# Optimization experiments

Measured on AMD Instinct MI355X. Metric: run time of the kernel, lower is better.

## Reference

```python
import jax, jax.numpy as jnp
import numpy as np
import math

B, H, S, D = 4, 16, 2048, 128

def setup_inputs() -> dict:
    key = jax.random.key(0)
    kq, kk, kv = jax.random.split(key, 3)
    query = jax.random.normal(kq, (B, H, S, D), dtype=jnp.float32)
    k = jax.random.normal(kk, (B, H, S, D), dtype=jnp.float32)
    value = jax.random.normal(kv, (B, H, S, D), dtype=jnp.float32)
    attn_mask = jnp.tril(jnp.ones((S, S), dtype=bool))  # causal
    key_padding_mask = jnp.ones((B, S), dtype=bool)      # all keys valid
    return {"query": query, "key": k, "value": value,
            "attn_mask": attn_mask, "key_padding_mask": key_padding_mask}

def reference(query, key, value, attn_mask, key_padding_mask):
    dk = query.shape[-1]
    # [B,H,Sq,Sk]
    scores = jnp.einsum('bhqd,bhkd->bhqk', query, key) / math.sqrt(dk)
    fill = jnp.finfo(scores.dtype).min
    # attn_mask [Sq,Sk] -> [1,1,Sq,Sk]; True = keep
    scores = jnp.where(attn_mask[None, None, :, :], scores, fill)
    # key_padding_mask [B,Sk] -> [B,1,1,Sk]; True = keep
    scores = jnp.where(key_padding_mask[:, None, None, :], scores, fill)
    attn = jax.nn.softmax(scores, axis=-1)
    # dropout p=0.0 / eval mode -> identity
    return jnp.einsum('bhqk,bhkd->bhqd', attn, value)
```

## Files before the change

### kernel.cpp

```cpp
#include <hip/hip_runtime.h>
#include <hip/hip_bf16.h>
#include <math.h>

#define S_LEN 2048
#define D_DIM 128
#define NHEADS 64

typedef unsigned short u16;
typedef __attribute__((ext_vector_type(8))) short bf16x8;
typedef __attribute__((ext_vector_type(4))) float f32x4;
typedef __attribute__((ext_vector_type(16))) float f32x16;

__device__ __forceinline__ u16 f2b(float f) {
  union { float f; unsigned u; } v; v.f = f;
  return (u16)((v.u + 0x7fffu + ((v.u >> 16) & 1u)) >> 16);
}
__device__ __forceinline__ unsigned cvtpk(float lo, float hi) {
  unsigned r;
  asm("v_cvt_pk_bf16_f32 %0, %1, %2" : "=v"(r) : "v"(lo), "v"(hi));
  return r;
}
__device__ __forceinline__ void pl32swap(unsigned &a, unsigned &b) {
  asm("v_permlane32_swap_b32 %0, %1" : "+v"(a), "+v"(b));
}
__device__ __forceinline__ f32x16 z16() {
  f32x16 v;
  #pragma unroll
  for (int i = 0; i < 16; ++i) v[i] = 0.f;
  return v;
}

#define GLL16(g, l) __builtin_amdgcn_global_load_lds(                       \
    (const __attribute__((address_space(1))) unsigned*)(g),                 \
    (__attribute__((address_space(3))) unsigned*)(l), 16, 0, 0)

__global__ __launch_bounds__(256, 2)
void conv_kernel(const float* __restrict__ K, const float* __restrict__ V,
                 u16* __restrict__ Kws, u16* __restrict__ Vws) {
  __shared__ float VLf[128 * 65];
  const int h = blockIdx.x >> 3;
  const int s = blockIdx.x & 7;
  const int tid = threadIdx.x;
  const size_t hb = (size_t)h * S_LEN * D_DIM;
  const float* Kb = K + hb;
  const float* Vb = V + hb;
  u16* Ko = Kws + hb;
  u16* Vo = Vws + hb;

  #pragma unroll 2
  for (int it = 0; it < 16; ++it) {
    int idx = it * 256 + tid;
    int k = 256 * s + (idx >> 4), g = idx & 15;
    const float* src = Kb + (size_t)k * D_DIM + 8 * g;
    float4 a = *(const float4*)src;
    float4 b = *(const float4*)(src + 4);
    bf16x8 f;
    f[0]=f2b(a.x); f[1]=f2b(a.y); f[2]=f2b(a.z); f[3]=f2b(a.w);
    f[4]=f2b(b.x); f[5]=f2b(b.y); f[6]=f2b(b.z); f[7]=f2b(b.w);
    *(bf16x8*)&Ko[(size_t)k * D_DIM + 8 * g] = f;
  }
  for (int tt = 0; tt < 4; ++tt) {
    const int k0t = 256 * s + 64 * tt;
    __syncthreads();
    #pragma unroll 2
    for (int it = 0; it < 8; ++it) {
      int idx = it * 256 + tid;
      int row = idx >> 5, c4 = idx & 31;
      float4 v = *(const float4*)(Vb + (size_t)(k0t + row) * D_DIM + 4 * c4);
      VLf[(4*c4 + 0) * 65 + row] = v.x;
      VLf[(4*c4 + 1) * 65 + row] = v.y;
      VLf[(4*c4 + 2) * 65 + row] = v.z;
      VLf[(4*c4 + 3) * 65 + row] = v.w;
    }
    __syncthreads();
    #pragma unroll
    for (int it = 0; it < 4; ++it) {
      int idx = it * 256 + tid;
      int d = idx >> 3, kc = idx & 7;
      const float* src = &VLf[d * 65 + 8 * kc];
      bf16x8 f;
      #pragma unroll
      for (int j = 0; j < 8; ++j) f[j] = f2b(src[j]);
      *(bf16x8*)&Vo[(size_t)d * S_LEN + k0t + 8 * kc] = f;
    }
  }
}

__global__ __launch_bounds__(512, 2)
void fattn8w(const float* __restrict__ Qg, const u16* __restrict__ Kws,
             const u16* __restrict__ Vws, float* __restrict__ Og) {
  __shared__ __align__(16) u16 Kl[3][8192];
  __shared__ __align__(16) u16 Vl[3][8192];

  const int tid = threadIdx.x, lane = tid & 63, w = tid >> 6;
  const int l31 = lane & 31, hi = lane >> 5;
  const int kx = l31 & 7;

  const int L = blockIdx.x;
  const int xcd = L & 7, slot = L >> 3;
  const int head = xcd * 8 + (slot >> 2);
  const int pr = slot & 3;

  const size_t hb = (size_t)head * S_LEN * D_DIM;
  const float* Qb = Qg + hb;
  float*       Ob = Og + hb;
  const u16*   Kh = Kws + hb;
  const u16*   Vh = Vws + hb;

  auto stage = [&](int buf, int t) {
    const int k0 = t * 64;
    #pragma unroll
    for (int j = 0; j < 2; ++j) {
      const int sb = (w * 2 + j) * 64;
      {
        int sk = sb + lane;
        int k = sk >> 4, gs = sk & 15, g = gs ^ (k & 7);
        GLL16(Kh + (size_t)(k0 + k) * D_DIM + 8 * g, &Kl[buf][sb * 8]);
      }
      {
        int sv = sb + lane;
        int d = sv >> 3, gks = sv & 7, gk = gks ^ (d & 7);
        GLL16(Vh + (size_t)d * S_LEN + k0 + 8 * gk, &Vl[buf][sb * 8]);
      }
    }
  };

#define CHUNK(SV, CB, CI)                                                   \
  do {                                                                      \
    float p0 = exp2f((SV)[(CB)+0] - m_run), p1 = exp2f((SV)[(CB)+1] - m_run); \
    float p2 = exp2f((SV)[(CB)+2] - m_run), p3 = exp2f((SV)[(CB)+3] - m_run); \
    float p4 = exp2f((SV)[(CB)+4] - m_run), p5 = exp2f((SV)[(CB)+5] - m_run); \
    float p6 = exp2f((SV)[(CB)+6] - m_run), p7 = exp2f((SV)[(CB)+7] - m_run); \
    psA += (p0 + p1) + (p2 + p3);                                           \
    psB += (p4 + p5) + (p6 + p7);                                           \
    unsigned a0 = cvtpk(p0, p1), a1 = cvtpk(p2, p3);                        \
    unsigned a2 = cvtpk(p4, p5), a3 = cvtpk(p6, p7);                        \
    pl32swap(a0, a2); pl32swap(a1, a3);                                     \
    union { unsigned u[4]; bf16x8 v; } pf_;                                 \
    pf_.u[0] = a0; pf_.u[1] = a1; pf_.u[2] = a2; pf_.u[3] = a3;             \
    const int gv = ((CI) * 2 + hi) ^ kx;                                    \
    bf16x8 v0 = *(const bf16x8*)&V8[( l31      ) * 64 + gv * 8];            \
    bf16x8 v1 = *(const bf16x8*)&V8[( 32 + l31 ) * 64 + gv * 8];            \
    bf16x8 v2 = *(const bf16x8*)&V8[( 64 + l31 ) * 64 + gv * 8];            \
    bf16x8 v3 = *(const bf16x8*)&V8[( 96 + l31 ) * 64 + gv * 8];            \
    __builtin_amdgcn_s_setprio(1);                                          \
    oa0 = __builtin_amdgcn_mfma_f32_32x32x16_bf16(v0, pf_.v, oa0, 0,0,0);   \
    oa1 = __builtin_amdgcn_mfma_f32_32x32x16_bf16(v1, pf_.v, oa1, 0,0,0);   \
    oa2 = __builtin_amdgcn_mfma_f32_32x32x16_bf16(v2, pf_.v, oa2, 0,0,0);   \
    oa3 = __builtin_amdgcn_mfma_f32_32x32x16_bf16(v3, pf_.v, oa3, 0,0,0);   \
    __builtin_amdgcn_s_setprio(0);                                          \
  } while (0)

  #pragma unroll 1
  for (int qi = 0; qi < 2; ++qi) {
    const int qt  = qi ? pr : (7 - pr);
    const int q0w = qt * 256 + 32 * w;
    const int ntk = 4 * qt + 4;
    const int myq = q0w + l31;

    bf16x8 qf[8];
    {
      const float sc = 0.12753139f;
      const float* qp = Qb + (size_t)myq * D_DIM + 8 * hi;
      #pragma unroll
      for (int c = 0; c < 8; ++c) {
        float4 a = *(const float4*)(qp + 16 * c);
        float4 b = *(const float4*)(qp + 16 * c + 4);
        bf16x8 f;
        f[0]=f2b(a.x*sc); f[1]=f2b(a.y*sc); f[2]=f2b(a.z*sc); f[3]=f2b(a.w*sc);
        f[4]=f2b(b.x*sc); f[5]=f2b(b.y*sc); f[6]=f2b(b.z*sc); f[7]=f2b(b.w*sc);
        qf[c] = f;
      }
    }

    f32x16 oa0 = z16(), oa1 = z16(), oa2 = z16(), oa3 = z16();
    float m_run = 0.f, l_run = 0.f;

    stage(0, 0);
    stage(1, 1);
    int rb = 0;

    #pragma unroll 1
    for (int t = 0; t < ntk; ++t) {
      if (t + 1 < ntk) asm volatile("s_waitcnt vmcnt(4)" ::: "memory");
      else             asm volatile("s_waitcnt vmcnt(0)" ::: "memory");
      __builtin_amdgcn_s_barrier();
      asm volatile("" ::: "memory");

      if (64 * t <= q0w + 31) {
        const u16* K8 = &Kl[rb][0];
        const u16* V8 = &Vl[rb][0];

        f32x16 s0 = z16(), s1 = z16();
        __builtin_amdgcn_s_setprio(1);
        #pragma unroll
        for (int c = 0; c < 8; ++c) {
          const int gs = (c * 2 + hi) ^ kx;
          bf16x8 ka = *(const bf16x8*)&K8[ l31       * 128 + gs * 8];
          bf16x8 kb = *(const bf16x8*)&K8[(32 + l31) * 128 + gs * 8];
          s0 = __builtin_amdgcn_mfma_f32_32x32x16_bf16(ka, qf[c], s0, 0,0,0);
          s1 = __builtin_amdgcn_mfma_f32_32x32x16_bf16(kb, qf[c], s1, 0,0,0);
        }
        __builtin_amdgcn_s_setprio(0);

        if (64 * t + 63 > q0w) {
          const int qm = myq - 64 * t;
          #pragma unroll
          for (int i = 0; i < 16; ++i) {
            const int kr = (i & 3) + 8 * (i >> 2) + 4 * hi;
            if (kr > qm)      s0[i] = -1e30f;
            if (32 + kr > qm) s1[i] = -1e30f;
          }
        }

        float tm[16];
        #pragma unroll
        for (int i = 0; i < 16; ++i) tm[i] = fmaxf(s0[i], s1[i]);
        #pragma unroll
        for (int st = 8; st >= 1; st >>= 1)
          #pragma unroll
          for (int i = 0; i < 8; ++i) if (i < st) tm[i] = fmaxf(tm[i], tm[i+st]);
        float mx = fmaxf(tm[0], __shfl_xor(tm[0], 32));

        if (mx > m_run + 8.0f) {
          float corr = exp2f(m_run - mx);
          #pragma unroll
          for (int i = 0; i < 16; ++i) {
            oa0[i] *= corr; oa1[i] *= corr; oa2[i] *= corr; oa3[i] *= corr;
          }
          l_run *= corr; m_run = mx;
        }

        float psA = 0.f, psB = 0.f;
        CHUNK(s0, 0, 0);
        CHUNK(s0, 8, 1);
        CHUNK(s1, 0, 2);
        CHUNK(s1, 8, 3);
        l_run += psA + psB;
      }

      if (t + 2 < ntk) {
        int nb = rb + 2; if (nb >= 3) nb -= 3;
        stage(nb, t + 2);
      }
      asm volatile("" ::: "memory");
      rb = (rb + 1 == 3) ? 0 : rb + 1;
    }

    float l_tot = l_run + __shfl_xor(l_run, 32);
    float inv = 1.0f / l_tot;
    float* op = Ob + (size_t)myq * D_DIM;
    #pragma unroll
    for (int i = 0; i < 16; ++i) {
      const int d = (i & 3) + 8 * (i >> 2) + 4 * hi;
      op[d]      = oa0[i] * inv;
      op[32 + d] = oa1[i] * inv;
      op[64 + d] = oa2[i] * inv;
      op[96 + d] = oa3[i] * inv;
    }
    __builtin_amdgcn_s_barrier();
  }
#undef CHUNK
}

__global__ __launch_bounds__(256, 3)
void fattn_v2(const float* __restrict__ Qg, const float* __restrict__ Kg,
              const float* __restrict__ Vg, float* __restrict__ Og) {
  __shared__ __align__(16) u16 K8[16 * 64 * 8];
  __shared__ __align__(16) u16 V8[8 * 128 * 8];
  __shared__ __align__(16) u16 Plf[4 * 16 * 72];
  const int tid = threadIdx.x, lane = tid & 63, w = tid >> 6;
  const int lr = lane & 15, lg = lane >> 4;
  const int qtile = blockIdx.x % 32, bh = blockIdx.x / 32;
  const int q0 = qtile * 64;
  const size_t base = (size_t)bh * S_LEN * D_DIM;
  const float *Qb = Qg + base, *Kb = Kg + base, *Vb = Vg + base;
  float* Ob = Og + base;
  bf16x8 qf[4];
  {
    const float* qp = Qb + (size_t)(q0 + w * 16 + lr) * D_DIM + lg * 8;
    #pragma unroll
    for (int cc = 0; cc < 4; ++cc) {
      float4 a = *(const float4*)(qp + cc * 32);
      float4 b = *(const float4*)(qp + cc * 32 + 4);
      bf16x8 f;
      f[0]=f2b(a.x); f[1]=f2b(a.y); f[2]=f2b(a.z); f[3]=f2b(a.w);
      f[4]=f2b(b.x); f[5]=f2b(b.y); f[6]=f2b(b.z); f[7]=f2b(b.w);
      qf[cc] = f;
    }
  }
  f32x4 oacc[8];
  #pragma unroll
  for (int c = 0; c < 8; ++c) oacc[c] = (f32x4){0.f,0.f,0.f,0.f};
  float m_run[4] = {-INFINITY,-INFINITY,-INFINITY,-INFINITY};
  float l_run[4] = {0.f,0.f,0.f,0.f};
  const int sg_ = tid >> 5, dq_ = tid & 31;
  float4 kb[8], vb[8];
  auto prefetch = [&](int k0) {
    const float* kp = Kb + (size_t)(k0 + lane) * D_DIM;
    #pragma unroll
    for (int i = 0; i < 4; ++i) {
      int dg = w + 4 * i;
      kb[2*i]   = *(const float4*)(kp + dg * 8);
      kb[2*i+1] = *(const float4*)(kp + dg * 8 + 4);
    }
    #pragma unroll
    for (int jj = 0; jj < 8; ++jj) {
      int row = k0 + (jj & 3) * 16 + 2 * sg_ + (jj >> 2);
      vb[jj] = *(const float4*)(Vb + (size_t)row * D_DIM + dq_ * 4);
    }
  };
  const int ntiles = qtile + 1;
  const float scale = 0.08838834764831845f;
  prefetch(0);
  for (int t = 0; t < ntiles; ++t) {
    #pragma unroll
    for (int i = 0; i < 4; ++i) {
      int dg = w + 4 * i;
      float4 a = kb[2*i], b = kb[2*i+1];
      bf16x8 f;
      f[0]=f2b(a.x); f[1]=f2b(a.y); f[2]=f2b(a.z); f[3]=f2b(a.w);
      f[4]=f2b(b.x); f[5]=f2b(b.y); f[6]=f2b(b.z); f[7]=f2b(b.w);
      *(bf16x8*)&K8[(dg * 64 + lane) * 8] = f;
    }
    #pragma unroll
    for (int dd = 0; dd < 4; ++dd) {
      bf16x8 f;
      #pragma unroll
      for (int jj = 0; jj < 8; ++jj) {
        float c = (dd==0)?vb[jj].x:(dd==1)?vb[jj].y:(dd==2)?vb[jj].z:vb[jj].w;
        f[jj] = f2b(c);
      }
      *(bf16x8*)&V8[(sg_ * 128 + dq_ * 4 + dd) * 8] = f;
    }
    __syncthreads();
    if (t + 1 < ntiles) prefetch((t + 1) * 64);
    const bool diag = (t == qtile);
    f32x4 sa[4];
    #pragma unroll
    for (int c = 0; c < 4; ++c) sa[c] = (f32x4){0.f,0.f,0.f,0.f};
    #pragma unroll
    for (int cc = 0; cc < 4; ++cc) {
      #pragma unroll
      for (int c = 0; c < 4; ++c) {
        bf16x8 kf = *(const bf16x8*)&K8[((cc*4+lg)*64 + c*16 + lr)*8];
        sa[c] = __builtin_amdgcn_mfma_f32_16x16x32_bf16(qf[cc], kf, sa[c], 0,0,0);
      }
    }
    #pragma unroll
    for (int r = 0; r < 4; ++r) {
      float s0=sa[0][r]*scale, s1=sa[1][r]*scale, s2=sa[2][r]*scale, s3=sa[3][r]*scale;
      if (diag) {
        int lim = 16*w + lg*4 + r;
        if (     lr > lim) s0 = -INFINITY;
        if (16 + lr > lim) s1 = -INFINITY;
        if (32 + lr > lim) s2 = -INFINITY;
        if (48 + lr > lim) s3 = -INFINITY;
      }
      float mx = fmaxf(fmaxf(s0,s1), fmaxf(s2,s3));
      #pragma unroll
      for (int d = 1; d < 16; d <<= 1) mx = fmaxf(mx, __shfl_xor(mx, d));
      float mn = fmaxf(m_run[r], mx);
      float corr = __expf(m_run[r] - mn);
      float p0=__expf(s0-mn), p1=__expf(s1-mn), p2=__expf(s2-mn), p3=__expf(s3-mn);
      float ps = (p0+p1)+(p2+p3);
      #pragma unroll
      for (int d = 1; d < 16; d <<= 1) ps += __shfl_xor(ps, d);
      l_run[r] = l_run[r]*corr + ps;
      m_run[r] = mn;
      #pragma unroll
      for (int c = 0; c < 8; ++c) oacc[c][r] *= corr;
      ushort4 pw = make_ushort4(f2b(p0), f2b(p1), f2b(p2), f2b(p3));
      *(ushort4*)&Plf[((w*16 + lg*4 + r) * 72) + 4*lr] = pw;
    }
    #pragma unroll
    for (int pass = 0; pass < 2; ++pass) {
      bf16x8 pfv = *(const bf16x8*)&Plf[(w*16 + lr)*72 + pass*32 + lg*8];
      #pragma unroll
      for (int c = 0; c < 8; ++c) {
        bf16x8 vf = *(const bf16x8*)&V8[((pass*4 + lg)*128 + c*16 + lr)*8];
        oacc[c] = __builtin_amdgcn_mfma_f32_16x16x32_bf16(pfv, vf, oacc[c], 0,0,0);
      }
    }
    __syncthreads();
  }
  #pragma unroll
  for (int r = 0; r < 4; ++r) {
    const int mq = q0 + w*16 + lg*4 + r;
    const float inv = 1.0f / l_run[r];
    float* op = Ob + (size_t)mq * D_DIM + lr;
    #pragma unroll
    for (int c = 0; c < 8; ++c) op[c*16] = oacc[c][r] * inv;
  }
}

extern "C" void kernel_launch(void* const* d_in, const int* in_sizes, int n_in,
                              void* d_out, int out_size, void* d_ws, size_t ws_size,
                              hipStream_t stream) {
  const float* Q = (const float*)d_in[0];
  const float* K = (const float*)d_in[1];
  const float* V = (const float*)d_in[2];
  float* O = (float*)d_out;
  const size_t elems = (size_t)NHEADS * S_LEN * D_DIM;
  const size_t need = 2 * elems * sizeof(u16);
  if (ws_size >= need) {
    u16* Kws = (u16*)d_ws;
    u16* Vws = Kws + elems;
    conv_kernel<<<dim3(512), dim3(256), 0, stream>>>(K, V, Kws, Vws);
    fattn8w<<<dim3(256), dim3(512), 0, stream>>>(Q, Kws, Vws, O);
  } else {
    fattn_v2<<<dim3(NHEADS * 32), dim3(256), 0, stream>>>(Q, K, V, O);
  }
}
```

Baseline: 147.6 us.

## Switch to double-buffered 128-key tiles with two 64-key subtiles per barrier

```diff
diff --git a/kernel.cpp b/kernel.cpp
--- a/kernel.cpp
+++ b/kernel.cpp
@@ -89,8 +89,8 @@
 __global__ __launch_bounds__(512, 2)
 void fattn8w(const float* __restrict__ Qg, const u16* __restrict__ Kws,
              const u16* __restrict__ Vws, float* __restrict__ Og) {
-  __shared__ __align__(16) u16 Kl[3][8192];
-  __shared__ __align__(16) u16 Vl[3][8192];
+  __shared__ __align__(16) u16 Kl[2][16384];
+  __shared__ __align__(16) u16 Vl[2][16384];
 
   const int tid = threadIdx.x, lane = tid & 63, w = tid >> 6;
   const int l31 = lane & 31, hi = lane >> 5;
@@ -108,10 +108,10 @@
   const u16*   Vh = Vws + hb;
 
   auto stage = [&](int buf, int t) {
-    const int k0 = t * 64;
-    #pragma unroll
-    for (int j = 0; j < 2; ++j) {
-      const int sb = (w * 2 + j) * 64;
+    const int k0 = t * 128;
+    #pragma unroll
+    for (int j = 0; j < 4; ++j) {
+      const int sb = (w * 4 + j) * 64;
       {
         int sk = sb + lane;
         int k = sk >> 4, gs = sk & 15, g = gs ^ (k & 7);
@@ -119,13 +119,13 @@
       }
       {
         int sv = sb + lane;
-        int d = sv >> 3, gks = sv & 7, gk = gks ^ (d & 7);
+        int d = sv >> 4, gks = sv & 15, gk = gks ^ (d & 7);
         GLL16(Vh + (size_t)d * S_LEN + k0 + 8 * gk, &Vl[buf][sb * 8]);
       }
     }
   };
 
-#define CHUNK(SV, CB, CI)                                                   \
+#define CHUNK(SV, CB, CI, TS)                                               \
   do {                                                                      \
     float p0 = exp2f((SV)[(CB)+0] - m_run), p1 = exp2f((SV)[(CB)+1] - m_run); \
     float p2 = exp2f((SV)[(CB)+2] - m_run), p3 = exp2f((SV)[(CB)+3] - m_run); \
@@ -138,11 +138,11 @@
     pl32swap(a0, a2); pl32swap(a1, a3);                                     \
     union { unsigned u[4]; bf16x8 v; } pf_;                                 \
     pf_.u[0] = a0; pf_.u[1] = a1; pf_.u[2] = a2; pf_.u[3] = a3;             \
-    const int gv = ((CI) * 2 + hi) ^ kx;                                    \
-    bf16x8 v0 = *(const bf16x8*)&V8[( l31      ) * 64 + gv * 8];            \
-    bf16x8 v1 = *(const bf16x8*)&V8[( 32 + l31 ) * 64 + gv * 8];            \
-    bf16x8 v2 = *(const bf16x8*)&V8[( 64 + l31 ) * 64 + gv * 8];            \
-    bf16x8 v3 = *(const bf16x8*)&V8[( 96 + l31 ) * 64 + gv * 8];            \
+    const int gv8 = (((CI) * 2 + hi) ^ kx) * 8 + (TS) * 64;                 \
+    bf16x8 v0 = *(const bf16x8*)&V8[( l31      ) * 128 + gv8];              \
+    bf16x8 v1 = *(const bf16x8*)&V8[( 32 + l31 ) * 128 + gv8];              \
+    bf16x8 v2 = *(const bf16x8*)&V8[( 64 + l31 ) * 128 + gv8];              \
+    bf16x8 v3 = *(const bf16x8*)&V8[( 96 + l31 ) * 128 + gv8];              \
     __builtin_amdgcn_s_setprio(1);                                          \
     oa0 = __builtin_amdgcn_mfma_f32_32x32x16_bf16(v0, pf_.v, oa0, 0,0,0);   \
     oa1 = __builtin_amdgcn_mfma_f32_32x32x16_bf16(v1, pf_.v, oa1, 0,0,0);   \
@@ -151,12 +151,63 @@
     __builtin_amdgcn_s_setprio(0);                                          \
   } while (0)
 
+#define SUBTILE(TS)                                                         \
+  do {                                                                      \
+    const int kk0 = 128 * t + 64 * (TS);                                    \
+    if (kk0 <= q0w + 31) {                                                  \
+      f32x16 s0 = z16(), s1 = z16();                                        \
+      __builtin_amdgcn_s_setprio(1);                                        \
+      _Pragma("unroll")                                                     \
+      for (int c = 0; c < 8; ++c) {                                         \
+        const int gs8 = ((c * 2 + hi) ^ kx) * 8;                            \
+        bf16x8 ka = *(const bf16x8*)&K8[(64*(TS)      + l31) * 128 + gs8];  \
+        bf16x8 kb = *(const bf16x8*)&K8[(64*(TS) + 32 + l31) * 128 + gs8];  \
+        s0 = __builtin_amdgcn_mfma_f32_32x32x16_bf16(ka, qf[c], s0, 0,0,0); \
+        s1 = __builtin_amdgcn_mfma_f32_32x32x16_bf16(kb, qf[c], s1, 0,0,0); \
+      }                                                                     \
+      __builtin_amdgcn_s_setprio(0);                                        \
+      if (kk0 + 63 > q0w) {                                                 \
+        const int qm = myq - kk0;                                           \
+        _Pragma("unroll")                                                   \
+        for (int i = 0; i < 16; ++i) {                                      \
+          const int kr = (i & 3) + 8 * (i >> 2) + 4 * hi;                   \
+          if (kr > qm)      s0[i] = -1e30f;                                 \
+          if (32 + kr > qm) s1[i] = -1e30f;                                 \
+        }                                                                   \
+      }                                                                     \
+      float tm[16];                                                         \
+      _Pragma("unroll")                                                     \
+      for (int i = 0; i < 16; ++i) tm[i] = fmaxf(s0[i], s1[i]);             \
+      _Pragma("unroll")                                                     \
+      for (int st = 8; st >= 1; st >>= 1)                                   \
+        _Pragma("unroll")                                                   \
+        for (int i = 0; i < 8; ++i) if (i < st) tm[i] = fmaxf(tm[i], tm[i+st]); \
+      float mx = fmaxf(tm[0], __shfl_xor(tm[0], 32));                       \
+      if (mx > m_run + 8.0f) {                     \
+        float corr = exp2f(m_run - mx);                                     \
+        _Pragma("unroll")                                                   \
+        for (int i = 0; i < 16; ++i) {                                      \
+          oa0[i] *= corr; oa1[i] *= corr; oa2[i] *= corr; oa3[i] *= corr;   \
+        }                                                                   \
+        l_run *= corr; m_run = mx;                                          \
+      }                                                                     \
+      float psA = 0.f, psB = 0.f;                                           \
+      CHUNK(s0, 0, 0, TS);                                                  \
+      CHUNK(s0, 8, 1, TS);                                                  \
+      CHUNK(s1, 0, 2, TS);                                                  \
+      CHUNK(s1, 8, 3, TS);                                                  \
+      l_run += psA + psB;                     \
+    }                                                                       \
+  } while (0)
+
   #pragma unroll 1
   for (int qi = 0; qi < 2; ++qi) {
     const int qt  = qi ? pr : (7 - pr);
     const int q0w = qt * 256 + 32 * w;
-    const int ntk = 4 * qt + 4;
+    const int nt  = 2 * qt + 2;
     const int myq = q0w + l31;
+
+    stage(0, 0);
 
     bf16x8 qf[8];
     {
@@ -176,90 +227,37 @@
     f32x16 oa0 = z16(), oa1 = z16(), oa2 = z16(), oa3 = z16();
     float m_run = 0.f, l_run = 0.f;
 
-    stage(0, 0);
-    stage(1, 1);
-    int rb = 0;
-
     #pragma unroll 1
-    for (int t = 0; t < ntk; ++t) {
-      if (t + 1 < ntk) asm volatile("s_waitcnt vmcnt(4)" ::: "memory");
-      else             asm volatile("s_waitcnt vmcnt(0)" ::: "memory");
+    for (int t = 0; t < nt; ++t) {
+      asm volatile("s_waitcnt vmcnt(0)" ::: "memory");
       __builtin_amdgcn_s_barrier();
       asm volatile("" ::: "memory");
-
-      if (64 * t <= q0w + 31) {
-        const u16* K8 = &Kl[rb][0];
-        const u16* V8 = &Vl[rb][0];
-
-        f32x16 s0 = z16(), s1 = z16();
-        __builtin_amdgcn_s_setprio(1);
-        #pragma unroll
-        for (int c = 0; c < 8; ++c) {
-          const int gs = (c * 2 + hi) ^ kx;
-          bf16x8 ka = *(const bf16x8*)&K8[ l31       * 128 + gs * 8];
-          bf16x8 kb = *(const bf16x8*)&K8[(32 + l31) * 128 + gs * 8];
-          s0 = __builtin_amdgcn_mfma_f32_32x32x16_bf16(ka, qf[c], s0, 0,0,0);
-          s1 = __builtin_amdgcn_mfma_f32_32x32x16_bf16(kb, qf[c], s1, 0,0,0);
-        }
-        __builtin_amdgcn_s_setprio(0);
-
-        if (64 * t + 63 > q0w) {
-          const int qm = myq - 64 * t;
-          #pragma unroll
-          for (int i = 0; i < 16; ++i) {
-            const int kr = (i & 3) + 8 * (i >> 2) + 4 * hi;
-            if (kr > qm)      s0[i] = -1e30f;
-            if (32 + kr > qm) s1[i] = -1e30f;
-          }
-        }
-
-        float tm[16];
-        #pragma unroll
-        for (int i = 0; i < 16; ++i) tm[i] = fmaxf(s0[i], s1[i]);
-        #pragma unroll
-        for (int st = 8; st >= 1; st >>= 1)
-          #pragma unroll
-          for (int i = 0; i < 8; ++i) if (i < st) tm[i] = fmaxf(tm[i], tm[i+st]);
-        float mx = fmaxf(tm[0], __shfl_xor(tm[0], 32));
-
-        if (mx > m_run + 8.0f) {
-          float corr = exp2f(m_run - mx);
-          #pragma unroll
-          for (int i = 0; i < 16; ++i) {
-            oa0[i] *= corr; oa1[i] *= corr; oa2[i] *= corr; oa3[i] *= corr;
-          }
-          l_run *= corr; m_run = mx;
-        }
-
-        float psA = 0.f, psB = 0.f;
-        CHUNK(s0, 0, 0);
-        CHUNK(s0, 8, 1);
-        CHUNK(s1, 0, 2);
-        CHUNK(s1, 8, 3);
-        l_run += psA + psB;
-      }
-
-      if (t + 2 < ntk) {
-        int nb = rb + 2; if (nb >= 3) nb -= 3;
-        stage(nb, t + 2);
-      }
-      asm volatile("" ::: "memory");
-      rb = (rb + 1 == 3) ? 0 : rb + 1;
+      if (t + 1 < nt) stage((t + 1) & 1, t + 1);
+
+      const u16* K8 = &Kl[t & 1][0];
+      const u16* V8 = &Vl[t & 1][0];
+      SUBTILE(0);
+      SUBTILE(1);
     }
 
     float l_tot = l_run + __shfl_xor(l_run, 32);
     float inv = 1.0f / l_tot;
     float* op = Ob + (size_t)myq * D_DIM;
     #pragma unroll
-    for (int i = 0; i < 16; ++i) {
-      const int d = (i & 3) + 8 * (i >> 2) + 4 * hi;
-      op[d]      = oa0[i] * inv;
-      op[32 + d] = oa1[i] * inv;
-      op[64 + d] = oa2[i] * inv;
-      op[96 + d] = oa3[i] * inv;
+    for (int b = 0; b < 4; ++b) {
+      const int d0 = 8 * b + 4 * hi;
+      *(float4*)(op + d0) =
+        make_float4(oa0[4*b]*inv, oa0[4*b+1]*inv, oa0[4*b+2]*inv, oa0[4*b+3]*inv);
+      *(float4*)(op + 32 + d0) =
+        make_float4(oa1[4*b]*inv, oa1[4*b+1]*inv, oa1[4*b+2]*inv, oa1[4*b+3]*inv);
+      *(float4*)(op + 64 + d0) =
+        make_float4(oa2[4*b]*inv, oa2[4*b+1]*inv, oa2[4*b+2]*inv, oa2[4*b+3]*inv);
+      *(float4*)(op + 96 + d0) =
+        make_float4(oa3[4*b]*inv, oa3[4*b+1]*inv, oa3[4*b+2]*inv, oa3[4*b+3]*inv);
     }
     __builtin_amdgcn_s_barrier();
   }
+#undef SUBTILE
 #undef CHUNK
 }
 
```

Result: slower. 157.3 us (+6.5%).

## Split paired causal q-tiles into separate blocks with double-buffered K/V staging

Applied to the files above, without the earlier changes.

```diff
diff --git a/kernel.cpp b/kernel.cpp
--- a/kernel.cpp
+++ b/kernel.cpp
@@ -89,17 +89,19 @@
 __global__ __launch_bounds__(512, 2)
 void fattn8w(const float* __restrict__ Qg, const u16* __restrict__ Kws,
              const u16* __restrict__ Vws, float* __restrict__ Og) {
-  __shared__ __align__(16) u16 Kl[3][8192];
-  __shared__ __align__(16) u16 Vl[3][8192];
+  __shared__ __align__(16) u16 Kl[2][8192];
+  __shared__ __align__(16) u16 Vl[2][8192];
 
   const int tid = threadIdx.x, lane = tid & 63, w = tid >> 6;
   const int l31 = lane & 31, hi = lane >> 5;
   const int kx = l31 & 7;
 
-  const int L = blockIdx.x;
-  const int xcd = L & 7, slot = L >> 3;
-  const int head = xcd * 8 + (slot >> 2);
-  const int pr = slot & 3;
+  const int b = blockIdx.x;
+  const int xcd = b & 7, slot = b >> 3;
+  const int head = xcd * 8 + (slot & 7);
+  const int qsel = slot >> 3;
+  const int qmap[8] = {7, 5, 6, 4, 0, 2, 1, 3};
+  const int qt = qmap[qsel];
 
   const size_t hb = (size_t)head * S_LEN * D_DIM;
   const float* Qb = Qg + hb;
@@ -151,114 +153,104 @@
     __builtin_amdgcn_s_setprio(0);                                          \
   } while (0)
 
+  const int q0w = qt * 256 + 32 * w;
+  const int ntk = 4 * qt + 4;
+  const int myq = q0w + l31;
+
+  stage(0, 0);
+
+  bf16x8 qf[8];
+  {
+    const float sc = 0.12753139f;
+    const float* qp = Qb + (size_t)myq * D_DIM + 8 * hi;
+    #pragma unroll
+    for (int c = 0; c < 8; ++c) {
+      float4 a = *(const float4*)(qp + 16 * c);
+      float4 b2 = *(const float4*)(qp + 16 * c + 4);
+      bf16x8 f;
+      f[0]=f2b(a.x*sc);  f[1]=f2b(a.y*sc);  f[2]=f2b(a.z*sc);  f[3]=f2b(a.w*sc);
+      f[4]=f2b(b2.x*sc); f[5]=f2b(b2.y*sc); f[6]=f2b(b2.z*sc); f[7]=f2b(b2.w*sc);
+      qf[c] = f;
+    }
+  }
+
+  f32x16 oa0 = z16(), oa1 = z16(), oa2 = z16(), oa3 = z16();
+  float m_run = 0.f, l_run = 0.f;
+
   #pragma unroll 1
-  for (int qi = 0; qi < 2; ++qi) {
-    const int qt  = qi ? pr : (7 - pr);
-    const int q0w = qt * 256 + 32 * w;
-    const int ntk = 4 * qt + 4;
-    const int myq = q0w + l31;
-
-    bf16x8 qf[8];
-    {
-      const float sc = 0.12753139f;
-      const float* qp = Qb + (size_t)myq * D_DIM + 8 * hi;
+  for (int t = 0; t < ntk; ++t) {
+    asm volatile("s_waitcnt vmcnt(0)" ::: "memory");
+    __builtin_amdgcn_s_barrier();
+    asm volatile("" ::: "memory");
+    if (t + 1 < ntk) stage((t + 1) & 1, t + 1);
+
+    if (64 * t <= q0w + 31) {
+      const u16* K8 = &Kl[t & 1][0];
+      const u16* V8 = &Vl[t & 1][0];
+
+      f32x16 s0 = z16(), s1 = z16();
+      __builtin_amdgcn_s_setprio(1);
       #pragma unroll
       for (int c = 0; c < 8; ++c) {
-        float4 a = *(const float4*)(qp + 16 * c);
-        float4 b = *(const float4*)(qp + 16 * c + 4);
-        bf16x8 f;
-        f[0]=f2b(a.x*sc); f[1]=f2b(a.y*sc); f[2]=f2b(a.z*sc); f[3]=f2b(a.w*sc);
-        f[4]=f2b(b.x*sc); f[5]=f2b(b.y*sc); f[6]=f2b(b.z*sc); f[7]=f2b(b.w*sc);
-        qf[c] = f;
-      }
-    }
-
-    f32x16 oa0 = z16(), oa1 = z16(), oa2 = z16(), oa3 = z16();
-    float m_run = 0.f, l_run = 0.f;
-
-    stage(0, 0);
-    stage(1, 1);
-    int rb = 0;
-
-    #pragma unroll 1
-    for (int t = 0; t < ntk; ++t) {
-      if (t + 1 < ntk) asm volatile("s_waitcnt vmcnt(4)" ::: "memory");
-      else             asm volatile("s_waitcnt vmcnt(0)" ::: "memory");
-      __builtin_amdgcn_s_barrier();
-      asm volatile("" ::: "memory");
-
-      if (64 * t <= q0w + 31) {
-        const u16* K8 = &Kl[rb][0];
-        const u16* V8 = &Vl[rb][0];
-
-        f32x16 s0 = z16(), s1 = z16();
-        __builtin_amdgcn_s_setprio(1);
+        const int gs = (c * 2 + hi) ^ kx;
+        bf16x8 ka = *(const bf16x8*)&K8[ l31       * 128 + gs * 8];
+        bf16x8 kb = *(const bf16x8*)&K8[(32 + l31) * 128 + gs * 8];
+        s0 = __builtin_amdgcn_mfma_f32_32x32x16_bf16(ka, qf[c], s0, 0,0,0);
+        s1 = __builtin_amdgcn_mfma_f32_32x32x16_bf16(kb, qf[c], s1, 0,0,0);
+      }
+      __builtin_amdgcn_s_setprio(0);
+
+      if (64 * t + 63 > q0w) {
+        const int qm = myq - 64 * t;
         #pragma unroll
-        for (int c = 0; c < 8; ++c) {
-          const int gs = (c * 2 + hi) ^ kx;
-          bf16x8 ka = *(const bf16x8*)&K8[ l31       * 128 + gs * 8];
-          bf16x8 kb = *(const bf16x8*)&K8[(32 + l31) * 128 + gs * 8];
-          s0 = __builtin_amdgcn_mfma_f32_32x32x16_bf16(ka, qf[c], s0, 0,0,0);
-          s1 = __builtin_amdgcn_mfma_f32_32x32x16_bf16(kb, qf[c], s1, 0,0,0);
+        for (int i = 0; i < 16; ++i) {
+          const int kr = (i & 3) + 8 * (i >> 2) + 4 * hi;
+          if (kr > qm)      s0[i] = -1e30f;
+          if (32 + kr > qm) s1[i] = -1e30f;
         }
-        __builtin_amdgcn_s_setprio(0);
-
-        if (64 * t + 63 > q0w) {
-          const int qm = myq - 64 * t;
-          #pragma unroll
-          for (int i = 0; i < 16; ++i) {
-            const int kr = (i & 3) + 8 * (i >> 2) + 4 * hi;
-            if (kr > qm)      s0[i] = -1e30f;
-            if (32 + kr > qm) s1[i] = -1e30f;
-          }
+      }
+
+      float tm[16];
+      #pragma unroll
+      for (int i = 0; i < 16; ++i) tm[i] = fmaxf(s0[i], s1[i]);
+      #pragma unroll
+      for (int st = 8; st >= 1; st >>= 1)
+        #pragma unroll
+        for (int i = 0; i < 8; ++i) if (i < st) tm[i] = fmaxf(tm[i], tm[i+st]);
+      float mx = fmaxf(tm[0], __shfl_xor(tm[0], 32));
+
+      if (mx > m_run + 8.0f) {
+        float corr = exp2f(m_run - mx);
+        #pragma unroll
+        for (int i = 0; i < 16; ++i) {
+          oa0[i] *= corr; oa1[i] *= corr; oa2[i] *= corr; oa3[i] *= corr;
         }
-
-        float tm[16];
-        #pragma unroll
-        for (int i = 0; i < 16; ++i) tm[i] = fmaxf(s0[i], s1[i]);
-        #pragma unroll
-        for (int st = 8; st >= 1; st >>= 1)
-          #pragma unroll
-          for (int i = 0; i < 8; ++i) if (i < st) tm[i] = fmaxf(tm[i], tm[i+st]);
-        float mx = fmaxf(tm[0], __shfl_xor(tm[0], 32));
-
-        if (mx > m_run + 8.0f) {
-          float corr = exp2f(m_run - mx);
-          #pragma unroll
-          for (int i = 0; i < 16; ++i) {
-            oa0[i] *= corr; oa1[i] *= corr; oa2[i] *= corr; oa3[i] *= corr;
-          }
-          l_run *= corr; m_run = mx;
-        }
-
-        float psA = 0.f, psB = 0.f;
-        CHUNK(s0, 0, 0);
-        CHUNK(s0, 8, 1);
-        CHUNK(s1, 0, 2);
-        CHUNK(s1, 8, 3);
-        l_run += psA + psB;
-      }
-
-      if (t + 2 < ntk) {
-        int nb = rb + 2; if (nb >= 3) nb -= 3;
-        stage(nb, t + 2);
-      }
-      asm volatile("" ::: "memory");
-      rb = (rb + 1 == 3) ? 0 : rb + 1;
-    }
-
-    float l_tot = l_run + __shfl_xor(l_run, 32);
-    float inv = 1.0f / l_tot;
-    float* op = Ob + (size_t)myq * D_DIM;
-    #pragma unroll
-    for (int i = 0; i < 16; ++i) {
-      const int d = (i & 3) + 8 * (i >> 2) + 4 * hi;
-      op[d]      = oa0[i] * inv;
-      op[32 + d] = oa1[i] * inv;
-      op[64 + d] = oa2[i] * inv;
-      op[96 + d] = oa3[i] * inv;
-    }
-    __builtin_amdgcn_s_barrier();
+        l_run *= corr; m_run = mx;
+      }
+
+      float psA = 0.f, psB = 0.f;
+      CHUNK(s0, 0, 0);
+      CHUNK(s0, 8, 1);
+      CHUNK(s1, 0, 2);
+      CHUNK(s1, 8, 3);
+      l_run += psA + psB;
+    }
+  }
+
+  float l_tot = l_run + __shfl_xor(l_run, 32);
+  float inv = 1.0f / l_tot;
+  float* op = Ob + (size_t)myq * D_DIM;
+  #pragma unroll
+  for (int bq = 0; bq < 4; ++bq) {
+    const int d0 = 8 * bq + 4 * hi;
+    *(float4*)(op + d0) =
+      make_float4(oa0[4*bq]*inv, oa0[4*bq+1]*inv, oa0[4*bq+2]*inv, oa0[4*bq+3]*inv);
+    *(float4*)(op + 32 + d0) =
+      make_float4(oa1[4*bq]*inv, oa1[4*bq+1]*inv, oa1[4*bq+2]*inv, oa1[4*bq+3]*inv);
+    *(float4*)(op + 64 + d0) =
+      make_float4(oa2[4*bq]*inv, oa2[4*bq+1]*inv, oa2[4*bq+2]*inv, oa2[4*bq+3]*inv);
+    *(float4*)(op + 96 + d0) =
+      make_float4(oa3[4*bq]*inv, oa3[4*bq+1]*inv, oa3[4*bq+2]*inv, oa3[4*bq+3]*inv);
   }
 #undef CHUNK
 }
@@ -407,7 +399,7 @@
     u16* Kws = (u16*)d_ws;
     u16* Vws = Kws + elems;
     conv_kernel<<<dim3(512), dim3(256), 0, stream>>>(K, V, Kws, Vws);
-    fattn8w<<<dim3(256), dim3(512), 0, stream>>>(Q, Kws, Vws, O);
+    fattn8w<<<dim3(512), dim3(512), 0, stream>>>(Q, Kws, Vws, O);
   } else {
     fattn_v2<<<dim3(NHEADS * 32), dim3(256), 0, stream>>>(Q, K, V, O);
   }
```

Result: slower. 172.4 us (+16.8%).
